# Optimization experiments

Hardware: AMD Instinct MI355X
Metric: run time of the kernel (lower is better)

## Reference

```python
import jax, jax.numpy as jnp
import numpy as np

D, M, ALPHA = 64, 512, 7.18
DIM = 1024
B = M * D  # batch: M clusters x D samples each


def setup_inputs() -> dict:
    key = jax.random.key(0)
    outputs = jax.random.normal(key, (B, DIM), dtype=jnp.float32)
    indices = jnp.arange(B, dtype=jnp.int64 if jax.config.jax_enable_x64 else jnp.int32)
    assignment = indices // D  # sample i -> cluster i//D (contiguous blocks of D)
    loss_vector = jnp.zeros((M,), jnp.float32)
    loss_count = jnp.zeros((M,), jnp.float32)
    return {"outputs": outputs, "indices": indices, "assignment": assignment,
            "loss_vector": loss_vector, "loss_count": loss_count}


def reference(outputs, indices, assignment, loss_vector, loss_count):
    outputs = outputs.astype(jnp.float32)
    own = assignment[indices]                              # [B] cluster id per sample
    n = jnp.float32(B)
    # cluster means (each cluster has exactly D samples)
    means = jax.ops.segment_sum(outputs, own, num_segments=M) / D   # [M, DIM]
    # pooled variance: sum ||x_i - mu_{c(i)}||^2 / (N - 1)
    diff_own = outputs - means[own]
    var_sum = jnp.sum(diff_own * diff_own)
    stdev = -2.0 * var_sum / (n - 1.0)                     # the (negative) -2*sigma^2 term
    # squared distances to every cluster mean: [B, M]
    sq = (jnp.sum(outputs * outputs, axis=1)[:, None]
          + jnp.sum(means * means, axis=1)[None, :]
          - 2.0 * outputs @ means.T)
    exps = jnp.exp(sq / stdev)                             # [B, M]
    own_col = own[:, None]
    own_exp = jnp.take_along_axis(exps, own_col, axis=1)[:, 0]
    denom = jnp.sum(exps, axis=1) - own_exp                # sum over mF != own
    sq_own = jnp.take_along_axis(sq, own_col, axis=1)[:, 0]
    log_ratio = sq_own / stdev - ALPHA - jnp.log(denom)    # log(exp(.-alpha)/denom)
    per_loss = jnp.maximum(-log_ratio, 0.0)                # == -clamp(log_ratio, max=0)
    loss = (jnp.sum(per_loss) / n).reshape(1)
    lv = (loss_vector + jax.ops.segment_sum(per_loss, own, num_segments=M)) / n
    lc = loss_count + jax.ops.segment_sum(jnp.ones((B,), jnp.float32), own, num_segments=M)
    variance = var_sum / (n - 1.0)                         # stdev / -2.0 in the original
    return loss, lv, lc, variance
```

## Files before the change

### kernel.cpp

```cpp
#include <hip/hip_runtime.h>
#include <hip/hip_bf16.h>
#include <stdint.h>

#define DIM 1024
#define ALPHA 7.18f
#define INV_N (1.0f/32768.0f)
#define NM1 32767.0f
#define LOG2E 1.44269504088896f
#define LN2 0.693147180559945f

typedef __attribute__((ext_vector_type(8))) short bfrag8;
typedef __attribute__((ext_vector_type(4))) float f32x4;

typedef const __attribute__((address_space(1))) void gv_t;
typedef __attribute__((address_space(3))) void lv_t;

__device__ __forceinline__ unsigned f2bf_bits(float f) {
    unsigned u = __float_as_uint(f);
    return (u + 0x7fffu + ((u >> 16) & 1u)) >> 16;
}

__global__ __launch_bounds__(512)
void k1_colsum(const float* __restrict__ outputs, const int* __restrict__ indices,
               const int* __restrict__ assignment, float* __restrict__ mean_sums,
               unsigned* __restrict__ counts, float* __restrict__ scalars,
               int* __restrict__ own_g, unsigned short* __restrict__ a_bf) {
    __shared__ int sown[64];
    __shared__ int suni;
    __shared__ float4 spart[256];
    __shared__ float ssq[8];
    const int tid = threadIdx.x;
    const int blk = blockIdx.x;
    const int row0 = blk * 64;
    if (tid == 0) suni = 1;
    if (tid < 64) {
        int m = assignment[indices[row0 + tid]];
        sown[tid] = m;
        own_g[row0 + tid] = m;
        atomicAdd(&counts[m], 1u);
    }
    __syncthreads();
    if (tid < 63 && sown[tid] != sown[tid + 1]) suni = 0;
    __syncthreads();

    const int c4 = tid & 255, rh = tid >> 8;
    const float* gp = outputs + (size_t)(row0 + rh) * DIM + c4 * 4;
    const int kc = (c4 >> 1) & 3, half = c4 & 1;
    char* abase = (char*)a_bf + (size_t)blk * 131072 + (c4 >> 3) * 4096 + half * 8;

    float4 s4 = {0.f, 0.f, 0.f, 0.f};
    float sq = 0.f;

    if (suni) {
        #pragma unroll 1
        for (int sb = 0; sb < 8; ++sb) {
            float4 v[4];
            #pragma unroll
            for (int r = 0; r < 4; ++r)
                v[r] = *(const float4*)(gp + (size_t)(sb * 8 + r * 2) * DIM);
            #pragma unroll
            for (int r = 0; r < 4; ++r) {
                sq = fmaf(v[r].x, v[r].x, sq); sq = fmaf(v[r].y, v[r].y, sq);
                sq = fmaf(v[r].z, v[r].z, sq); sq = fmaf(v[r].w, v[r].w, sq);
                s4.x += v[r].x; s4.y += v[r].y; s4.z += v[r].z; s4.w += v[r].w;
                int rr = sb * 8 + r * 2 + rh;
                unsigned lo = f2bf_bits(v[r].x) | (f2bf_bits(v[r].y) << 16);
                unsigned hi = f2bf_bits(v[r].z) | (f2bf_bits(v[r].w) << 16);
                *(uint2*)(abase + rr * 64 + ((kc ^ ((rr >> 1) & 3)) << 4)) = make_uint2(lo, hi);
            }
        }
        if (rh) spart[c4] = s4;
        __syncthreads();
        if (!rh) {
            float4 o = spart[c4];
            float* dst = mean_sums + (size_t)sown[0] * DIM + c4 * 4;
            atomicAdd(dst + 0, s4.x + o.x); atomicAdd(dst + 1, s4.y + o.y);
            atomicAdd(dst + 2, s4.z + o.z); atomicAdd(dst + 3, s4.w + o.w);
        }
    } else {
        int curm = sown[rh];
        for (int r = 0; r < 32; ++r) {
            int rr = r * 2 + rh;
            float4 v = *(const float4*)(gp + (size_t)(r * 2) * DIM);
            int m = sown[rr];
            if (m != curm) {
                float* dst = mean_sums + (size_t)curm * DIM + c4 * 4;
                atomicAdd(dst + 0, s4.x); atomicAdd(dst + 1, s4.y);
                atomicAdd(dst + 2, s4.z); atomicAdd(dst + 3, s4.w);
                s4 = (float4){0.f, 0.f, 0.f, 0.f};
                curm = m;
            }
            sq = fmaf(v.x, v.x, sq); sq = fmaf(v.y, v.y, sq);
            sq = fmaf(v.z, v.z, sq); sq = fmaf(v.w, v.w, sq);
            s4.x += v.x; s4.y += v.y; s4.z += v.z; s4.w += v.w;
            unsigned lo = f2bf_bits(v.x) | (f2bf_bits(v.y) << 16);
            unsigned hi = f2bf_bits(v.z) | (f2bf_bits(v.w) << 16);
            *(uint2*)(abase + rr * 64 + ((kc ^ ((rr >> 1) & 3)) << 4)) = make_uint2(lo, hi);
        }
        float* dst = mean_sums + (size_t)curm * DIM + c4 * 4;
        atomicAdd(dst + 0, s4.x); atomicAdd(dst + 1, s4.y);
        atomicAdd(dst + 2, s4.z); atomicAdd(dst + 3, s4.w);
        __syncthreads();
    }

    #pragma unroll
    for (int mk = 32; mk; mk >>= 1) sq += __shfl_xor(sq, mk, 64);
    if ((tid & 63) == 0) ssq[tid >> 6] = sq;
    __syncthreads();
    if (tid == 0) {
        float s = 0.f;
        #pragma unroll
        for (int w = 0; w < 8; ++w) s += ssq[w];
        atomicAdd(&scalars[0], s);
    }
}

__global__ __launch_bounds__(256)
void k2_means(const float* __restrict__ mean_sums, const unsigned* __restrict__ counts,
              unsigned short* __restrict__ b_kt, float* __restrict__ msq,
              float* __restrict__ scalars) {
    const int m = blockIdx.x, t = threadIdx.x;
    const float* row = mean_sums + (size_t)m * DIM;
    float4 v = *(const float4*)(row + t * 4);
    float4 mu = {v.x * (1.0f/64.0f), v.y * (1.0f/64.0f), v.z * (1.0f/64.0f), v.w * (1.0f/64.0f)};
    const int tt = t >> 3, kc = (t >> 1) & 3, half = t & 1;
    unsigned lo = f2bf_bits(mu.x) | (f2bf_bits(mu.y) << 16);
    unsigned hi = f2bf_bits(mu.z) | (f2bf_bits(mu.w) << 16);
    *(uint2*)((char*)b_kt + tt * 32768 + m * 64 + ((kc ^ ((m >> 1) & 3)) << 4) + half * 8)
        = make_uint2(lo, hi);
    float sq = fmaf(mu.x, mu.x, fmaf(mu.y, mu.y, fmaf(mu.z, mu.z, mu.w * mu.w)));
    #pragma unroll
    for (int mk = 32; mk; mk >>= 1) sq += __shfl_xor(sq, mk, 64);
    __shared__ float sw[4];
    if ((t & 63) == 0) sw[t >> 6] = sq;
    __syncthreads();
    if (t == 0) {
        float s = sw[0] + sw[1] + sw[2] + sw[3];
        msq[m] = s;
        atomicAdd(&scalars[1], ((float)counts[m] - 128.0f) * s);
    }
}

__global__ __launch_bounds__(512)
void k3_finalize(float* __restrict__ scalars, const float* __restrict__ msq,
                 const unsigned* __restrict__ counts, const float* __restrict__ loss_vector,
                 const float* __restrict__ loss_count, float* __restrict__ msl,
                 float* __restrict__ out) {
    const int t = threadIdx.x;
    float var_sum = scalars[0] + scalars[1];
    float inv_std = -NM1 / (2.0f * var_sum);
    msl[t] = msq[t] * inv_std * LOG2E;
    out[1 + t] = loss_vector[t] * INV_N;
    out[513 + t] = loss_count[t] + (float)counts[t];
    if (t == 0) {
        out[0] = 0.0f;
        out[1025] = var_sum / NM1;
        scalars[2] = inv_std;
    }
}

#define K4_STAGE(s, lab, lbb) do {                                             \
    const char* _gb = bbase + (size_t)(s) * 32768 + (wid * 4) * 1024 + lane * 16; \
    _Pragma("unroll")                                                          \
    for (int _i = 0; _i < 4; ++_i)                                             \
        __builtin_amdgcn_global_load_lds((gv_t*)(_gb + _i * 1024),             \
                                         (lv_t*)((lbb) + (wid * 4 + _i) * 1024), 16, 0, 0); \
    if (wid < 4) {                                                             \
        const char* _ga = aprime + (size_t)(s) * 4096 + wid * 1024 + lane * 16; \
        __builtin_amdgcn_global_load_lds((gv_t*)_ga, (lv_t*)((lab) + wid * 1024), 16, 0, 0); \
    }                                                                          \
} while (0)

#define K4_COMPUTE(lab, lbb) do {                                              \
    const char* pa = (lab) + ar_byte;                                          \
    const char* pb = (lbb) + br_byte;                                          \
    bfrag8 a0 = *(const bfrag8*)(pa);                                          \
    bfrag8 a1 = *(const bfrag8*)(pa + 1024);                                   \
    _Pragma("unroll")                                                          \
    for (int fn = 0; fn < 8; ++fn) {                                           \
        bfrag8 bf = *(const bfrag8*)(pb + fn * 1024);                          \
        acc[0][fn] = __builtin_amdgcn_mfma_f32_16x16x32_bf16(a0, bf, acc[0][fn], 0, 0, 0); \
        acc[1][fn] = __builtin_amdgcn_mfma_f32_16x16x32_bf16(a1, bf, acc[1][fn], 0, 0, 0); \
    }                                                                          \
} while (0)

__global__ __launch_bounds__(512)
void k4_gemm(const unsigned short* __restrict__ a_bf, const unsigned short* __restrict__ b_kt,
             const float* __restrict__ msl, const float* __restrict__ scalars,
             const int* __restrict__ own_g, float* __restrict__ out) {
    __shared__ short lA[3][64 * 32];
    __shared__ short lB[3][512 * 32];
    __shared__ float red_sum[64][4];
    __shared__ float red_own[64][4];

    const int tid  = threadIdx.x;
    const int lane = tid & 63;
    const int wid  = tid >> 6;
    const int wm   = wid >> 2;
    const int wn   = wid & 3;
    const int brow = blockIdx.x * 64;

    const int arow = wm * 32 + (lane & 15);
    const int ar_byte = arow * 64 + (((lane >> 4) ^ ((arow >> 1) & 3)) << 4);
    const int bcol = wn * 128 + (lane & 15);
    const int br_byte = bcol * 64 + (((lane >> 4) ^ ((bcol >> 1) & 3)) << 4);

    const char* aprime = (const char*)a_bf + (size_t)blockIdx.x * 131072;
    const char* bbase  = (const char*)b_kt;

    f32x4 acc[2][8];
    #pragma unroll
    for (int i = 0; i < 2; ++i)
        #pragma unroll
        for (int j = 0; j < 8; ++j)
            acc[i][j] = (f32x4){0.f, 0.f, 0.f, 0.f};

    char* la0 = (char*)&lA[0][0]; char* la1 = (char*)&lA[1][0]; char* la2 = (char*)&lA[2][0];
    char* lb0 = (char*)&lB[0][0]; char* lb1 = (char*)&lB[1][0]; char* lb2 = (char*)&lB[2][0];

    K4_STAGE(0, la0, lb0);
    K4_STAGE(1, la1, lb1);

    #pragma unroll 1
    for (int t = 0; t < 31; ++t) {
        if (wid < 4) asm volatile("s_waitcnt vmcnt(5) lgkmcnt(0)" ::: "memory");
        else         asm volatile("s_waitcnt vmcnt(4) lgkmcnt(0)" ::: "memory");
        __builtin_amdgcn_sched_barrier(0);
        __builtin_amdgcn_s_barrier();
        __builtin_amdgcn_sched_barrier(0);
        K4_COMPUTE(la0, lb0);
        if (t < 30) K4_STAGE(t + 2, la2, lb2);
        char* ta = la0; la0 = la1; la1 = la2; la2 = ta;
        char* tb = lb0; lb0 = lb1; lb1 = lb2; lb2 = tb;
    }
    asm volatile("s_waitcnt vmcnt(0) lgkmcnt(0)" ::: "memory");
    __builtin_amdgcn_sched_barrier(0);
    __builtin_amdgcn_s_barrier();
    __builtin_amdgcn_sched_barrier(0);
    K4_COMPUTE(la0, lb0);

    float mslv[8];
    #pragma unroll
    for (int fn = 0; fn < 8; ++fn) mslv[fn] = msl[bcol + fn * 16];
    const float inv_std = scalars[2];
    const float c2k = -2.0f * inv_std * LOG2E;
    int ownv[2][4];
    #pragma unroll
    for (int fm = 0; fm < 2; ++fm)
        #pragma unroll
        for (int rg = 0; rg < 4; ++rg)
            ownv[fm][rg] = own_g[brow + wm * 32 + fm * 16 + ((lane >> 4) << 2) + rg];

    #pragma unroll
    for (int fm = 0; fm < 2; ++fm) {
        #pragma unroll
        for (int rg = 0; rg < 4; ++rg) {
            float sum = 0.f, oa = -1e30f;
            int ownr = ownv[fm][rg];
            #pragma unroll
            for (int fn = 0; fn < 8; ++fn) {
                float dot = acc[fm][fn][rg];
                float arg = fmaf(c2k, dot, mslv[fn]);
                sum += exp2f(arg);
                bool isown = (bcol + fn * 16) == ownr;
                oa = isown ? arg : oa;
            }
            #pragma unroll
            for (int mk = 1; mk < 16; mk <<= 1) {
                sum += __shfl_xor(sum, mk, 64);
                oa = fmaxf(oa, __shfl_xor(oa, mk, 64));
            }
            if ((lane & 15) == 0) {
                int r_in = wm * 32 + fm * 16 + ((lane >> 4) << 2) + rg;
                red_sum[r_in][wn] = sum;
                red_own[r_in][wn] = oa;
            }
        }
    }
    __syncthreads();

    if (tid < 64) {
        float s = red_sum[tid][0] + red_sum[tid][1] + red_sum[tid][2] + red_sum[tid][3];
        float oa = fmaxf(fmaxf(red_own[tid][0], red_own[tid][1]),
                         fmaxf(red_own[tid][2], red_own[tid][3]));
        float denom = s - exp2f(oa);
        float per_loss = fmaxf(ALPHA + LN2 * (log2f(denom) - oa), 0.f);
        int ownr = own_g[brow + tid];
        float ls = per_loss;
        #pragma unroll
        for (int mk = 1; mk < 64; mk <<= 1) ls += __shfl_xor(ls, mk, 64);
        int own0 = __shfl(ownr, 0, 64);
        if (__all(ownr == own0)) {
            if (tid == 0) atomicAdd(&out[1 + own0], ls * INV_N);
        } else {
            atomicAdd(&out[1 + ownr], per_loss * INV_N);
        }
        if (tid == 0) atomicAdd(&out[0], ls * INV_N);
    }
}

extern "C" void kernel_launch(void* const* d_in, const int* in_sizes, int n_in,
                              void* d_out, int out_size, void* d_ws, size_t ws_size,
                              hipStream_t stream) {
    const float* outputs     = (const float*)d_in[0];
    const int*   indices     = (const int*)d_in[1];
    const int*   assignment  = (const int*)d_in[2];
    const float* loss_vector = (const float*)d_in[3];
    const float* loss_count  = (const float*)d_in[4];
    float* out = (float*)d_out;

    char* ws = (char*)d_ws;
    float*          mean_sums = (float*)ws;
    unsigned*       counts    = (unsigned*)(ws + 2097152);
    float*          scalars   = (float*)(ws + 2099200);
    const size_t    ZB        = 2099456;
    unsigned short* b_kt      = (unsigned short*)(ws + 2101248);
    float*          msq       = (float*)(ws + 3149824);
    float*          msl       = (float*)(ws + 3151872);
    int*            own_g     = (int*)(ws + 3153920);
    unsigned short* a_bf      = (unsigned short*)(ws + 4194304);

    hipMemsetAsync(d_ws, 0, ZB, stream);
    hipLaunchKernelGGL(k1_colsum, dim3(512), dim3(512), 0, stream,
                       outputs, indices, assignment, mean_sums, counts, scalars, own_g, a_bf);
    hipLaunchKernelGGL(k2_means, dim3(512), dim3(256), 0, stream,
                       mean_sums, counts, b_kt, msq, scalars);
    hipLaunchKernelGGL(k3_finalize, dim3(1), dim3(512), 0, stream,
                       scalars, msq, counts, loss_vector, loss_count, msl, out);
    hipLaunchKernelGGL(k4_gemm, dim3(512), dim3(512), 0, stream,
                       a_bf, b_kt, msl, scalars, own_g, out);
}
```

Baseline: 298.4 us.

## Split colsum kernel across column quarters with 4x more blocks

The first kernel now launches 2048 blocks: each 64-row group is split into four column quarters, and each block's 512 threads cover 8 row groups of 64 columns. Each thread issues all 8 row loads up front instead of looping over 8 sequential sub-batches, which exposes more memory-level parallelism and improves occupancy for the 128 MB read. The block-level reduction now goes through an 8-way shared array, and count and own_g updates are restricted to the cq==0 block. The sumsq atomic now fires from four times as many blocks, adding some contention.

```diff
diff --git a/kernel.cpp b/kernel.cpp
--- a/kernel.cpp
+++ b/kernel.cpp
@@ -27,77 +27,79 @@
                int* __restrict__ own_g, unsigned short* __restrict__ a_bf) {
     __shared__ int sown[64];
     __shared__ int suni;
-    __shared__ float4 spart[256];
+    __shared__ float4 spart[8][64];
     __shared__ float ssq[8];
     const int tid = threadIdx.x;
-    const int blk = blockIdx.x;
-    const int row0 = blk * 64;
+    const int rg = blockIdx.x >> 2, cq = blockIdx.x & 3;
+    const int row0 = rg * 64;
     if (tid == 0) suni = 1;
     if (tid < 64) {
         int m = assignment[indices[row0 + tid]];
         sown[tid] = m;
-        own_g[row0 + tid] = m;
-        atomicAdd(&counts[m], 1u);
+        if (cq == 0) { own_g[row0 + tid] = m; atomicAdd(&counts[m], 1u); }
     }
     __syncthreads();
     if (tid < 63 && sown[tid] != sown[tid + 1]) suni = 0;
     __syncthreads();
 
-    const int c4 = tid & 255, rh = tid >> 8;
-    const float* gp = outputs + (size_t)(row0 + rh) * DIM + c4 * 4;
-    const int kc = (c4 >> 1) & 3, half = c4 & 1;
-    char* abase = (char*)a_bf + (size_t)blk * 131072 + (c4 >> 3) * 4096 + half * 8;
+    const int ch = tid & 63;
+    const int rgrp = tid >> 6;
+    const int c = cq * 64 + ch;
+    const float* gp = outputs + (size_t)(row0 + rgrp * 8) * DIM + c * 4;
+    const int tt = c >> 3, kc = (c >> 1) & 3, half = c & 1;
+    char* abase = (char*)a_bf + (size_t)rg * 131072 + tt * 4096 + half * 8;
+
+    float4 v[8];
+    #pragma unroll
+    for (int r = 0; r < 8; ++r) v[r] = *(const float4*)(gp + (size_t)r * DIM);
 
     float4 s4 = {0.f, 0.f, 0.f, 0.f};
     float sq = 0.f;
 
     if (suni) {
-        #pragma unroll 1
-        for (int sb = 0; sb < 8; ++sb) {
-            float4 v[4];
+        #pragma unroll
+        for (int r = 0; r < 8; ++r) {
+            sq = fmaf(v[r].x, v[r].x, sq); sq = fmaf(v[r].y, v[r].y, sq);
+            sq = fmaf(v[r].z, v[r].z, sq); sq = fmaf(v[r].w, v[r].w, sq);
+            s4.x += v[r].x; s4.y += v[r].y; s4.z += v[r].z; s4.w += v[r].w;
+            int rr = rgrp * 8 + r;
+            unsigned lo = f2bf_bits(v[r].x) | (f2bf_bits(v[r].y) << 16);
+            unsigned hi = f2bf_bits(v[r].z) | (f2bf_bits(v[r].w) << 16);
+            *(uint2*)(abase + rr * 64 + ((kc ^ ((rr >> 1) & 3)) << 4)) = make_uint2(lo, hi);
+        }
+        if (rgrp) spart[rgrp][ch] = s4;
+        __syncthreads();
+        if (rgrp == 0) {
             #pragma unroll
-            for (int r = 0; r < 4; ++r)
-                v[r] = *(const float4*)(gp + (size_t)(sb * 8 + r * 2) * DIM);
-            #pragma unroll
-            for (int r = 0; r < 4; ++r) {
-                sq = fmaf(v[r].x, v[r].x, sq); sq = fmaf(v[r].y, v[r].y, sq);
-                sq = fmaf(v[r].z, v[r].z, sq); sq = fmaf(v[r].w, v[r].w, sq);
-                s4.x += v[r].x; s4.y += v[r].y; s4.z += v[r].z; s4.w += v[r].w;
-                int rr = sb * 8 + r * 2 + rh;
-                unsigned lo = f2bf_bits(v[r].x) | (f2bf_bits(v[r].y) << 16);
-                unsigned hi = f2bf_bits(v[r].z) | (f2bf_bits(v[r].w) << 16);
-                *(uint2*)(abase + rr * 64 + ((kc ^ ((rr >> 1) & 3)) << 4)) = make_uint2(lo, hi);
-            }
-        }
-        if (rh) spart[c4] = s4;
-        __syncthreads();
-        if (!rh) {
-            float4 o = spart[c4];
-            float* dst = mean_sums + (size_t)sown[0] * DIM + c4 * 4;
-            atomicAdd(dst + 0, s4.x + o.x); atomicAdd(dst + 1, s4.y + o.y);
-            atomicAdd(dst + 2, s4.z + o.z); atomicAdd(dst + 3, s4.w + o.w);
+            for (int r = 1; r < 8; ++r) {
+                float4 o = spart[r][ch];
+                s4.x += o.x; s4.y += o.y; s4.z += o.z; s4.w += o.w;
+            }
+            float* dst = mean_sums + (size_t)sown[0] * DIM + c * 4;
+            atomicAdd(dst + 0, s4.x); atomicAdd(dst + 1, s4.y);
+            atomicAdd(dst + 2, s4.z); atomicAdd(dst + 3, s4.w);
         }
     } else {
-        int curm = sown[rh];
-        for (int r = 0; r < 32; ++r) {
-            int rr = r * 2 + rh;
-            float4 v = *(const float4*)(gp + (size_t)(r * 2) * DIM);
+        int curm = sown[rgrp * 8];
+        #pragma unroll
+        for (int r = 0; r < 8; ++r) {
+            int rr = rgrp * 8 + r;
             int m = sown[rr];
             if (m != curm) {
-                float* dst = mean_sums + (size_t)curm * DIM + c4 * 4;
+                float* dst = mean_sums + (size_t)curm * DIM + c * 4;
                 atomicAdd(dst + 0, s4.x); atomicAdd(dst + 1, s4.y);
                 atomicAdd(dst + 2, s4.z); atomicAdd(dst + 3, s4.w);
                 s4 = (float4){0.f, 0.f, 0.f, 0.f};
                 curm = m;
             }
-            sq = fmaf(v.x, v.x, sq); sq = fmaf(v.y, v.y, sq);
-            sq = fmaf(v.z, v.z, sq); sq = fmaf(v.w, v.w, sq);
-            s4.x += v.x; s4.y += v.y; s4.z += v.z; s4.w += v.w;
-            unsigned lo = f2bf_bits(v.x) | (f2bf_bits(v.y) << 16);
-            unsigned hi = f2bf_bits(v.z) | (f2bf_bits(v.w) << 16);
+            sq = fmaf(v[r].x, v[r].x, sq); sq = fmaf(v[r].y, v[r].y, sq);
+            sq = fmaf(v[r].z, v[r].z, sq); sq = fmaf(v[r].w, v[r].w, sq);
+            s4.x += v[r].x; s4.y += v[r].y; s4.z += v[r].z; s4.w += v[r].w;
+            unsigned lo = f2bf_bits(v[r].x) | (f2bf_bits(v[r].y) << 16);
+            unsigned hi = f2bf_bits(v[r].z) | (f2bf_bits(v[r].w) << 16);
             *(uint2*)(abase + rr * 64 + ((kc ^ ((rr >> 1) & 3)) << 4)) = make_uint2(lo, hi);
         }
-        float* dst = mean_sums + (size_t)curm * DIM + c4 * 4;
+        float* dst = mean_sums + (size_t)curm * DIM + c * 4;
         atomicAdd(dst + 0, s4.x); atomicAdd(dst + 1, s4.y);
         atomicAdd(dst + 2, s4.z); atomicAdd(dst + 3, s4.w);
         __syncthreads();
@@ -321,7 +323,7 @@
     unsigned short* a_bf      = (unsigned short*)(ws + 4194304);
 
     hipMemsetAsync(d_ws, 0, ZB, stream);
-    hipLaunchKernelGGL(k1_colsum, dim3(512), dim3(512), 0, stream,
+    hipLaunchKernelGGL(k1_colsum, dim3(2048), dim3(512), 0, stream,
                        outputs, indices, assignment, mean_sums, counts, scalars, own_g, a_bf);
     hipLaunchKernelGGL(k2_means, dim3(512), dim3(256), 0, stream,
                        mean_sums, counts, b_kt, msq, scalars);
```

New measurement: 301.6 us. About the same (+1.1%).
